# Optimization experiments

Hardware: AMD Instinct MI355X
Metric: run time of the kernel (lower is better)

Reference implementation:

```python
import jax, jax.numpy as jnp
import numpy as np

N, E, H, L, IN, OUT = 50000, 800000, 64, 14, 128, 112
MSG_EPS = 1e-7   # GENConv message epsilon
LN_EPS = 1e-5    # torch.nn.LayerNorm default eps


def setup_inputs() -> dict:
    key = jax.random.key(0)
    ks = jax.random.split(key, 8)
    s = 0.05
    x = jax.random.normal(ks[0], (N, IN), jnp.float32)
    edge_index = jax.random.randint(ks[1], (2, E), 0, N, dtype=jnp.int64)
    enc_W = jax.random.normal(ks[2], (IN, H), jnp.float32) * s
    enc_b = jnp.zeros((H,), jnp.float32)
    ln_g = jnp.ones((L, H), jnp.float32)
    ln_b = jnp.zeros((L, H), jnp.float32)
    mlp_W = jax.random.normal(ks[3], (L, H, H), jnp.float32) * s
    mlp_b = jnp.zeros((L, H), jnp.float32)
    pred_W = jax.random.normal(ks[4], (H, OUT), jnp.float32) * s
    pred_b = jnp.zeros((OUT,), jnp.float32)
    return dict(x=x, edge_index=edge_index, enc_W=enc_W, enc_b=enc_b,
                ln_g=ln_g, ln_b=ln_b, mlp_W=mlp_W, mlp_b=mlp_b,
                pred_W=pred_W, pred_b=pred_b)


def _layernorm(h, g, b):
    mu = jnp.mean(h, axis=-1, keepdims=True)
    var = jnp.mean(jnp.square(h - mu), axis=-1, keepdims=True)  # biased, as torch
    return (h - mu) * jax.lax.rsqrt(var + LN_EPS) * g + b


def _genconv(h, src, dst, W, b):
    # GENConv: msg = relu(x_src) + eps; softmax aggregation (t=1) over dst; out = Linear(x + agg)
    msg = jax.nn.relu(h[src]) + MSG_EPS                    # [E, H]
    mmax = jax.ops.segment_max(msg, dst, num_segments=N)   # [N, H]
    mmax = jnp.where(jnp.isfinite(mmax), mmax, 0.0)         # empty segments
    ex = jnp.exp(msg - mmax[dst])                           # [E, H]
    denom = jax.ops.segment_sum(ex, dst, num_segments=N)    # [N, H]
    num = jax.ops.segment_sum(msg * ex, dst, num_segments=N)
    agg = num / jnp.maximum(denom, 1e-16)                   # 0 for isolated nodes
    return (h + agg) @ W + b


def reference(x, edge_index, enc_W, enc_b, ln_g, ln_b, mlp_W, mlp_b, pred_W, pred_b):
    src, dst = edge_index[0], edge_index[1]
    h = x @ enc_W + enc_b                       # node feature encoder
    h = _genconv(h, src, dst, mlp_W[0], mlp_b[0])  # first GCN (no pre-norm in res+)

    def body(h, params):
        g, bl, W, b = params
        h2 = jax.nn.relu(_layernorm(h, g, bl))  # dropout is identity (eval)
        h = _genconv(h2, src, dst, W, b) + h    # residual
        return h, None

    h, _ = jax.lax.scan(body, h, (ln_g[:L - 1], ln_b[:L - 1], mlp_W[1:], mlp_b[1:]))
    return h @ pred_W + pred_b
```

## Files before the change

### kernel.cpp

```cpp
#include <hip/hip_runtime.h>
#include <hip/hip_bf16.h>

#define NN 50000
#define EE 800000
#define HD 64
#define LL 14
#define IND 128
#define OUTD 112
#define LN2 0.69314718056f

typedef __attribute__((ext_vector_type(8))) short short8;
typedef __attribute__((ext_vector_type(4))) float float4_;
typedef __attribute__((ext_vector_type(4))) unsigned short ushort4_;

__device__ __forceinline__ short bf16_hi(float x) {
    return (short)(__float_as_uint(x) >> 16);
}
__device__ __forceinline__ float bf16_f(short s) {
    return __uint_as_float(((unsigned)(unsigned short)s) << 16);
}
__device__ __forceinline__ unsigned short f2b_rne(float x) {
    unsigned u = __float_as_uint(x);
    u += 0x7fffu + ((u >> 16) & 1u);
    return (unsigned short)(u >> 16);
}

__device__ __forceinline__ void split8(const float* p, short8& hi, short8& lo) {
    float4_ a = *(const float4_*)p;
    float4_ b = *(const float4_*)(p + 4);
    float v[8] = {a[0], a[1], a[2], a[3], b[0], b[1], b[2], b[3]};
    #pragma unroll
    for (int j = 0; j < 8; ++j) {
        short h = bf16_hi(v[j]);
        hi[j] = h;
        lo[j] = bf16_hi(v[j] - bf16_f(h));
    }
}

__device__ __forceinline__ void load_b(const float* __restrict__ W, int ldw,
                                       int colbase, int krow, short8& hi, short8& lo) {
    #pragma unroll
    for (int j = 0; j < 8; ++j) {
        float wv = W[(krow + j) * ldw + colbase];
        short h = bf16_hi(wv);
        hi[j] = h;
        lo[j] = bf16_hi(wv - bf16_f(h));
    }
}

__device__ __forceinline__ float4_ mm3(short8 ah, short8 al, short8 bh, short8 bl,
                                       float4_ acc) {
    acc = __builtin_amdgcn_mfma_f32_16x16x32_bf16(ah, bh, acc, 0, 0, 0);
    acc = __builtin_amdgcn_mfma_f32_16x16x32_bf16(al, bh, acc, 0, 0, 0);
    acc = __builtin_amdgcn_mfma_f32_16x16x32_bf16(ah, bl, acc, 0, 0, 0);
    return acc;
}

#define ACCQ(q, sv, nv) { \
    float p0_ = __uint_as_float((q).x << 16); \
    float p1_ = __uint_as_float((q).x & 0xffff0000u); \
    float p2_ = __uint_as_float((q).y << 16); \
    float p3_ = __uint_as_float((q).y & 0xffff0000u); \
    sv[0] += p0_; sv[1] += p1_; sv[2] += p2_; sv[3] += p3_; \
    nv[0] = fmaf(p0_, __log2f(fmaxf(p0_, 1e-20f)), nv[0]); \
    nv[1] = fmaf(p1_, __log2f(fmaxf(p1_, 1e-20f)), nv[1]); \
    nv[2] = fmaf(p2_, __log2f(fmaxf(p2_, 1e-20f)), nv[2]); \
    nv[3] = fmaf(p3_, __log2f(fmaxf(p3_, 1e-20f)), nv[3]); }


__global__ void k_hist(const int* __restrict__ ei, int* __restrict__ cnt,
                       int* __restrict__ rank) {
    int e = blockIdx.x * blockDim.x + threadIdx.x;
    if (e < EE) rank[e] = atomicAdd(&cnt[ei[EE + e]], 1);
}

__global__ __launch_bounds__(1024) void k_scan1(const int* __restrict__ deg,
                                                int* __restrict__ excl,
                                                int* __restrict__ bsum) {
    __shared__ int ws[16];
    int tid = threadIdx.x, lane = tid & 63, w = tid >> 6;
    int gid = blockIdx.x * 1024 + tid;
    int v = (gid < NN) ? deg[gid] : 0;
    int x = v;
    #pragma unroll
    for (int d = 1; d < 64; d <<= 1) {
        int y = __shfl_up(x, d);
        if (lane >= d) x += y;
    }
    if (lane == 63) ws[w] = x;
    __syncthreads();
    if (tid == 0) {
        int acc = 0;
        for (int i = 0; i < 16; i++) { int t = ws[i]; ws[i] = acc; acc += t; }
        bsum[blockIdx.x] = acc;
    }
    __syncthreads();
    if (gid < NN) excl[gid] = x - v + ws[w];
}

__global__ void k_scan2(const int* __restrict__ bsum, int* __restrict__ boff, int nb) {
    if (threadIdx.x == 0) {
        int acc = 0;
        for (int i = 0; i < nb; i++) { boff[i] = acc; acc += bsum[i]; }
    }
}

__global__ __launch_bounds__(1024) void k_scan3(int* __restrict__ rp,
                                                const int* __restrict__ boff) {
    int gid = blockIdx.x * 1024 + threadIdx.x;
    if (gid < NN) rp[gid] += boff[blockIdx.x];
    if (gid == 0) rp[NN] = EE;
}

__global__ void k_scatter(const int* __restrict__ ei, const int* __restrict__ rp,
                          const int* __restrict__ rank, int* __restrict__ csrc) {
    int e = blockIdx.x * blockDim.x + threadIdx.x;
    if (e < EE) {
        int d = ei[EE + e];
        csrc[rp[d] + rank[e]] = ei[e];
    }
}


__global__ __launch_bounds__(256) void k_enc(const float* __restrict__ x,
                                             const float* __restrict__ W,
                                             const float* __restrict__ b,
                                             float* __restrict__ h,
                                             unsigned short* __restrict__ P0,
                                             unsigned short* __restrict__ P1) {
    __shared__ float X[16 * 132];
    int tid = threadIdx.x, lane = tid & 63, w = tid >> 6;
    int nb = blockIdx.x * 16;
    int nq = lane >> 4, nr = lane & 15;
    int colbase = w * 16 + nr;

    if (blockIdx.x == 0 && tid < HD) {
        P0[(size_t)NN * HD + tid] = 0;
        P1[(size_t)NN * HD + tid] = 0;
    }

    {
        const float* src = x + (size_t)nb * IND + tid * 8;
        float4_ a = *(const float4_*)src;
        float4_ c = *(const float4_*)(src + 4);
        int m = tid >> 4, k8 = 8 * (tid & 15);
        *(float4_*)&X[m * 132 + k8] = a;
        *(float4_*)&X[m * 132 + k8 + 4] = c;
    }
    __syncthreads();

    float4_ acc = {};
    #pragma unroll
    for (int t = 0; t < 4; ++t) {
        short8 ah, al, bh, bl;
        split8(&X[nr * 132 + t * 32 + nq * 8], ah, al);
        load_b(W, HD, colbase, t * 32 + nq * 8, bh, bl);
        acc = mm3(ah, al, bh, bl, acc);
    }

    float bias = b[colbase];
    #pragma unroll
    for (int r = 0; r < 4; ++r) {
        int node = nb + nq * 4 + r;
        float y = acc[r] + bias;
        h[node * HD + colbase] = y;
        float msg = fminf(fmaxf(y, 0.f) + 1e-7f, 50.f);
        P0[node * HD + colbase] = f2b_rne(__expf(msg));
    }
}

__device__ __forceinline__ void gtail(const unsigned* __restrict__ Pb,
                                      const int* __restrict__ csrc,
                                      int beg, int deg, int g, int co, int lane,
                                      float4_& sv, float4_& nv) {
    for (int chunk = 64; chunk < deg; chunk += 64) {
        int my = (chunk + lane < deg) ? csrc[beg + chunk + lane] : NN;
        int cnt = min(64, deg - chunk);
        int nb4 = (cnt + 3) >> 2;
        for (int k = 0; k < nb4; ++k) {
            int e = __shfl(my, k * 4 + g);
            uint2 q = *(const uint2*)(Pb + (((unsigned)e) << 5) + co);
            ACCQ(q, sv, nv);
        }
    }
}

__device__ __forceinline__ void finish_node(float4_ sv, float4_ nv, int node, int row,
                                            int g, int ci, int co,
                                            const float* __restrict__ selfh,
                                            const unsigned* __restrict__ Pb,
                                            uint2 selfq, float* __restrict__ T) {
    float t0 = sv[0], t1 = sv[1], t2 = sv[2], t3 = sv[3];
    float u0 = nv[0], u1 = nv[1], u2 = nv[2], u3 = nv[3];
    #pragma unroll
    for (int d = 16; d < 64; d <<= 1) {
        t0 += __shfl_xor(t0, d); t1 += __shfl_xor(t1, d);
        t2 += __shfl_xor(t2, d); t3 += __shfl_xor(t3, d);
        u0 += __shfl_xor(u0, d); u1 += __shfl_xor(u1, d);
        u2 += __shfl_xor(u2, d); u3 += __shfl_xor(u3, d);
    }
    if (g == 0) {
        float a0 = LN2 * u0 / fmaxf(t0, 1e-16f);
        float a1 = LN2 * u1 / fmaxf(t1, 1e-16f);
        float a2 = LN2 * u2 / fmaxf(t2, 1e-16f);
        float a3 = LN2 * u3 / fmaxf(t3, 1e-16f);
        float4_ xv;
        if (selfh) {
            float4_ sf = *(const float4_*)&selfh[(size_t)node * HD + ci * 4];
            xv[0] = sf[0] + a0; xv[1] = sf[1] + a1;
            xv[2] = sf[2] + a2; xv[3] = sf[3] + a3;
        } else {
            unsigned d0 = selfq.x, d1 = selfq.y;
            xv[0] = LN2 * __log2f(__uint_as_float(d0 << 16)) - 1e-7f + a0;
            xv[1] = LN2 * __log2f(__uint_as_float(d0 & 0xffff0000u)) - 1e-7f + a1;
            xv[2] = LN2 * __log2f(__uint_as_float(d1 << 16)) - 1e-7f + a2;
            xv[3] = LN2 * __log2f(__uint_as_float(d1 & 0xffff0000u)) - 1e-7f + a3;
        }
        *(float4_*)&T[row * 68 + ci * 4] = xv;
    }
}

__global__ __launch_bounds__(256, 4) void k_layer(const unsigned short* __restrict__ Pin,
                                                  const float* __restrict__ selfh,
                                                  const float* __restrict__ hres,
                                                  float* __restrict__ hout,
                                                  unsigned short* __restrict__ Pout,
                                                  const int* __restrict__ rp,
                                                  const int* __restrict__ csrc,
                                                  const float* __restrict__ W,
                                                  const float* __restrict__ b,
                                                  const float* __restrict__ gnext,
                                                  const float* __restrict__ bnext) {
    __shared__ float T[16 * 68];
    int tid = threadIdx.x, lane = tid & 63, w = tid >> 6;
    int nb = blockIdx.x * 16;
    int nq = lane >> 4, nr = lane & 15;
    int colbase = w * 16 + nr;

    short8 Bhi[2], Blo[2];
    #pragma unroll
    for (int t = 0; t < 2; ++t)
        load_b(W, HD, colbase, t * 32 + nq * 8, Bhi[t], Blo[t]);

    int g = lane >> 4;
    int ci = lane & 15;
    int co = ci << 1;
    int node0 = nb + w * 4;
    const unsigned* Pb = (const unsigned*)Pin;

    int r0 = rp[node0], r1 = rp[node0 + 1], r2 = rp[node0 + 2],
        r3 = rp[node0 + 3], r4 = rp[node0 + 4];
    int dA = r1 - r0, dB = r2 - r1, dC = r3 - r2, dD = r4 - r3;

    int myA = (lane < dA) ? csrc[r0 + lane] : NN;
    int myB = (lane < dB) ? csrc[r1 + lane] : NN;
    int myC = (lane < dC) ? csrc[r2 + lane] : NN;
    int myD = (lane < dD) ? csrc[r3 + lane] : NN;

    uint2 sq0 = {0, 0}, sq1 = {0, 0}, sq2 = {0, 0}, sq3 = {0, 0};
    if (!selfh) {
        sq0 = *(const uint2*)(Pb + (((unsigned)(node0 + 0)) << 5) + co);
        sq1 = *(const uint2*)(Pb + (((unsigned)(node0 + 1)) << 5) + co);
        sq2 = *(const uint2*)(Pb + (((unsigned)(node0 + 2)) << 5) + co);
        sq3 = *(const uint2*)(Pb + (((unsigned)(node0 + 3)) << 5) + co);
    }

    int cA = min(dA, 64), cB = min(dB, 64), cC = min(dC, 64), cD = min(dD, 64);
    int nk = (max(max(cA, cB), max(cC, cD)) + 3) >> 2;

    float4_ sA = {}, nA = {}, sB = {}, nB = {}, sC = {}, nC = {}, sD = {}, nD = {};

    #pragma unroll 2
    for (int k = 0; k < nk; ++k) {
        int sidx = k * 4 + g;
        int e0 = __shfl(myA, sidx);
        int e1 = __shfl(myB, sidx);
        int e2 = __shfl(myC, sidx);
        int e3 = __shfl(myD, sidx);
        uint2 q0 = *(const uint2*)(Pb + (((unsigned)e0) << 5) + co);
        uint2 q1 = *(const uint2*)(Pb + (((unsigned)e1) << 5) + co);
        uint2 q2 = *(const uint2*)(Pb + (((unsigned)e2) << 5) + co);
        uint2 q3 = *(const uint2*)(Pb + (((unsigned)e3) << 5) + co);
        ACCQ(q0, sA, nA);
        ACCQ(q1, sB, nB);
        ACCQ(q2, sC, nC);
        ACCQ(q3, sD, nD);
    }
    if (dA > 64) gtail(Pb, csrc, r0, dA, g, co, lane, sA, nA);
    if (dB > 64) gtail(Pb, csrc, r1, dB, g, co, lane, sB, nB);
    if (dC > 64) gtail(Pb, csrc, r2, dC, g, co, lane, sC, nC);
    if (dD > 64) gtail(Pb, csrc, r3, dD, g, co, lane, sD, nD);

    finish_node(sA, nA, node0 + 0, w * 4 + 0, g, ci, co, selfh, Pb, sq0, T);
    finish_node(sB, nB, node0 + 1, w * 4 + 1, g, ci, co, selfh, Pb, sq1, T);
    finish_node(sC, nC, node0 + 2, w * 4 + 2, g, ci, co, selfh, Pb, sq2, T);
    finish_node(sD, nD, node0 + 3, w * 4 + 3, g, ci, co, selfh, Pb, sq3, T);
    __syncthreads();

    short8 Ahi[2], Alo[2];
    #pragma unroll
    for (int t = 0; t < 2; ++t)
        split8(&T[nr * 68 + t * 32 + nq * 8], Ahi[t], Alo[t]);
    __syncthreads();

    float4_ acc = {};
    #pragma unroll
    for (int t = 0; t < 2; ++t)
        acc = mm3(Ahi[t], Alo[t], Bhi[t], Blo[t], acc);

    float bias = b[colbase];
    #pragma unroll
    for (int r = 0; r < 4; ++r) {
        int m = nq * 4 + r;
        int node = nb + m;
        float v = acc[r] + bias;
        if (hres) v += hres[node * HD + colbase];
        hout[node * HD + colbase] = v;
        T[m * 68 + colbase] = v;
    }
    if (!Pout) return;
    __syncthreads();

    int m = tid >> 4, c4 = (tid & 15) * 4;
    float4_ vv = *(const float4_*)&T[m * 68 + c4];
    float ps_ = (vv[0] + vv[1]) + (vv[2] + vv[3]);
    float pq_ = (vv[0] * vv[0] + vv[1] * vv[1]) + (vv[2] * vv[2] + vv[3] * vv[3]);
    #pragma unroll
    for (int d = 8; d; d >>= 1) {
        ps_ += __shfl_xor(ps_, d);
        pq_ += __shfl_xor(pq_, d);
    }
    float mu = ps_ * (1.f / 64.f);
    float var = pq_ * (1.f / 64.f) - mu * mu;
    float inv = rsqrtf(fmaxf(var, 0.f) + 1e-5f);
    float4_ g4 = *(const float4_*)&gnext[c4];
    float4_ b4 = *(const float4_*)&bnext[c4];
    ushort4_ po;
    #pragma unroll
    for (int j = 0; j < 4; ++j) {
        float y = fmaxf((vv[j] - mu) * inv * g4[j] + b4[j], 0.f);
        float msg = fminf(y + 1e-7f, 50.f);
        po[j] = f2b_rne(__expf(msg));
    }
    *(ushort4_*)&Pout[(nb + m) * HD + c4] = po;
}


__global__ __launch_bounds__(256) void k_pred(const float* __restrict__ h,
                                              const float* __restrict__ W,
                                              const float* __restrict__ b,
                                              float* __restrict__ out) {
    __shared__ float T[16 * 68];
    int tid = threadIdx.x, lane = tid & 63, w = tid >> 6;
    int nb = blockIdx.x * 16;
    int nq = lane >> 4, nr = lane & 15;

    {
        const float* src = h + (size_t)nb * HD + tid * 4;
        float4_ a = *(const float4_*)src;
        int m = tid >> 4, k4 = 4 * (tid & 15);
        *(float4_*)&T[m * 68 + k4] = a;
    }
    __syncthreads();

    short8 Ahi[2], Alo[2];
    #pragma unroll
    for (int t = 0; t < 2; ++t)
        split8(&T[nr * 68 + t * 32 + nq * 8], Ahi[t], Alo[t]);

    for (int tt = w; tt < 7; tt += 4) {
        int colbase = tt * 16 + nr;
        float4_ acc = {};
        #pragma unroll
        for (int t = 0; t < 2; ++t) {
            short8 bh, bl;
            load_b(W, OUTD, colbase, t * 32 + nq * 8, bh, bl);
            acc = mm3(Ahi[t], Alo[t], bh, bl, acc);
        }
        float bias = b[colbase];
        #pragma unroll
        for (int r = 0; r < 4; ++r) {
            int node = nb + nq * 4 + r;
            out[node * OUTD + colbase] = acc[r] + bias;
        }
    }
}


extern "C" void kernel_launch(void* const* d_in, const int* in_sizes, int n_in,
                              void* d_out, int out_size, void* d_ws, size_t ws_size,
                              hipStream_t stream) {
    const float* x    = (const float*)d_in[0];
    const int*   ei   = (const int*)d_in[1];
    const float* encW = (const float*)d_in[2];
    const float* encb = (const float*)d_in[3];
    const float* lng  = (const float*)d_in[4];
    const float* lnb  = (const float*)d_in[5];
    const float* mlpW = (const float*)d_in[6];
    const float* mlpb = (const float*)d_in[7];
    const float* pW   = (const float*)d_in[8];
    const float* pb   = (const float*)d_in[9];
    float* out = (float*)d_out;

    float* hA  = (float*)d_ws;
    float* hB  = hA + (size_t)NN * HD;
    unsigned short* PA = (unsigned short*)(hB + (size_t)NN * HD);
    unsigned short* PB = PA + (size_t)(NN + 1) * HD;
    int* rp   = (int*)(PB + (size_t)(NN + 1) * HD);
    int* cnt  = rp + (NN + 1);
    int* csrc = cnt + NN;
    int* rank = csrc + EE;
    int* bsum = rank + EE;
    int* boff = bsum + 64;

    hipMemsetAsync(cnt, 0, NN * sizeof(int), stream);
    k_hist<<<(EE + 255) / 256, 256, 0, stream>>>(ei, cnt, rank);
    const int NB = (NN + 1023) / 1024;
    k_scan1<<<NB, 1024, 0, stream>>>(cnt, rp, bsum);
    k_scan2<<<1, 64, 0, stream>>>(bsum, boff, NB);
    k_scan3<<<NB, 1024, 0, stream>>>(rp, boff);
    k_scatter<<<(EE + 255) / 256, 256, 0, stream>>>(ei, rp, rank, csrc);

    k_enc<<<NN / 16, 256, 0, stream>>>(x, encW, encb, hA, PA, PB);

    k_layer<<<NN / 16, 256, 0, stream>>>(PA, hA, nullptr, hB, PB, rp, csrc,
                                         mlpW, mlpb, lng, lnb);

    float* hres = hB;
    float* hdst = hA;
    unsigned short* pc = PB;
    unsigned short* pn = PA;
    for (int l = 1; l < LL; ++l) {
        bool last = (l == LL - 1);
        k_layer<<<NN / 16, 256, 0, stream>>>(pc, nullptr, hres, hdst,
                                             last ? nullptr : pn,
                                             rp, csrc,
                                             mlpW + (size_t)l * HD * HD,
                                             mlpb + (size_t)l * HD,
                                             last ? nullptr : lng + (size_t)l * HD,
                                             last ? nullptr : lnb + (size_t)l * HD);
        float* t = hres; hres = hdst; hdst = t;
        unsigned short* u = pc; pc = pn; pn = u;
    }

    k_pred<<<NN / 16, 256, 0, stream>>>(hres, pW, pb, out);
}
```

Measured before the change: 696.7 us.

## Sort nodes by in-degree to balance per-wave gather work

Adds a counting-sort pass (histogram, scan, scatter) that orders nodes by in-degree, capped at 63, into a descriptor array. Each layer wave then processes four nodes of similar degree, so lanes waste fewer iterations padding to the largest degree in the group. The padding sentinel row now holds exp(0)=1, so the log guard can be dropped, and that padding is subtracted from the denominator. The block-offset scan also becomes a wave shuffle scan. In exchange, outputs are written through an indirect node index, so stores scatter instead of being contiguous, and three small setup kernels are added.

Result: faster. 671.3 us (-3.7%).

```diff
diff --git a/kernel.cpp b/kernel.cpp
--- a/kernel.cpp
+++ b/kernel.cpp
@@ -62,10 +62,10 @@
     float p2_ = __uint_as_float((q).y << 16); \
     float p3_ = __uint_as_float((q).y & 0xffff0000u); \
     sv[0] += p0_; sv[1] += p1_; sv[2] += p2_; sv[3] += p3_; \
-    nv[0] = fmaf(p0_, __log2f(fmaxf(p0_, 1e-20f)), nv[0]); \
-    nv[1] = fmaf(p1_, __log2f(fmaxf(p1_, 1e-20f)), nv[1]); \
-    nv[2] = fmaf(p2_, __log2f(fmaxf(p2_, 1e-20f)), nv[2]); \
-    nv[3] = fmaf(p3_, __log2f(fmaxf(p3_, 1e-20f)), nv[3]); }
+    nv[0] = fmaf(p0_, __log2f(p0_), nv[0]); \
+    nv[1] = fmaf(p1_, __log2f(p1_), nv[1]); \
+    nv[2] = fmaf(p2_, __log2f(p2_), nv[2]); \
+    nv[3] = fmaf(p3_, __log2f(p3_), nv[3]); }
 
 
 __global__ void k_hist(const int* __restrict__ ei, int* __restrict__ cnt,
@@ -99,10 +99,15 @@
 }
 
 __global__ void k_scan2(const int* __restrict__ bsum, int* __restrict__ boff, int nb) {
-    if (threadIdx.x == 0) {
-        int acc = 0;
-        for (int i = 0; i < nb; i++) { boff[i] = acc; acc += bsum[i]; }
-    }
+    int lane = threadIdx.x & 63;
+    int v = (lane < nb) ? bsum[lane] : 0;
+    int x = v;
+    #pragma unroll
+    for (int d = 1; d < 64; d <<= 1) {
+        int y = __shfl_up(x, d);
+        if (lane >= d) x += y;
+    }
+    if (lane < nb) boff[lane] = x - v;
 }
 
 __global__ __launch_bounds__(1024) void k_scan3(int* __restrict__ rp,
@@ -118,6 +123,54 @@
     if (e < EE) {
         int d = ei[EE + e];
         csrc[rp[d] + rank[e]] = ei[e];
+    }
+}
+
+
+__global__ __launch_bounds__(256) void k_dhist(const int* __restrict__ deg,
+                                               int* __restrict__ bhist) {
+    __shared__ int lh[64];
+    int tid = threadIdx.x;
+    if (tid < 64) lh[tid] = 0;
+    __syncthreads();
+    int n = blockIdx.x * 256 + tid;
+    if (n < NN) atomicAdd(&lh[min(deg[n], 63)], 1);
+    __syncthreads();
+    if (tid < 64 && lh[tid]) atomicAdd(&bhist[tid], lh[tid]);
+}
+
+__global__ void k_dscan(const int* __restrict__ bhist, int* __restrict__ gboff) {
+    int lane = threadIdx.x & 63;
+    int v = bhist[lane];
+    int x = v;
+    #pragma unroll
+    for (int d = 1; d < 64; d <<= 1) {
+        int y = __shfl_up(x, d);
+        if (lane >= d) x += y;
+    }
+    gboff[lane] = x - v;
+}
+
+__global__ __launch_bounds__(256) void k_dscatter(const int* __restrict__ deg,
+                                                  const int* __restrict__ rp,
+                                                  int* __restrict__ gboff,
+                                                  int4* __restrict__ nd) {
+    __shared__ int lh[64], lbase[64];
+    int tid = threadIdx.x;
+    if (tid < 64) lh[tid] = 0;
+    __syncthreads();
+    int n = blockIdx.x * 256 + tid;
+    int b = 0, lr = 0;
+    if (n < NN) {
+        b = min(deg[n], 63);
+        lr = atomicAdd(&lh[b], 1);
+    }
+    __syncthreads();
+    if (tid < 64) lbase[tid] = lh[tid] ? atomicAdd(&gboff[tid], lh[tid]) : 0;
+    __syncthreads();
+    if (n < NN) {
+        int pos = lbase[b] + lr;
+        nd[pos] = make_int4(n, rp[n], rp[n + 1] - rp[n], 0);
     }
 }
 
@@ -135,8 +188,8 @@
     int colbase = w * 16 + nr;
 
     if (blockIdx.x == 0 && tid < HD) {
-        P0[(size_t)NN * HD + tid] = 0;
-        P1[(size_t)NN * HD + tid] = 0;
+        P0[(size_t)NN * HD + tid] = 0x3f80;
+        P1[(size_t)NN * HD + tid] = 0x3f80;
     }
 
     {
@@ -172,11 +225,12 @@
 __device__ __forceinline__ void gtail(const unsigned* __restrict__ Pb,
                                       const int* __restrict__ csrc,
                                       int beg, int deg, int g, int co, int lane,
-                                      float4_& sv, float4_& nv) {
+                                      float4_& sv, float4_& nv, int& waste) {
     for (int chunk = 64; chunk < deg; chunk += 64) {
         int my = (chunk + lane < deg) ? csrc[beg + chunk + lane] : NN;
         int cnt = min(64, deg - chunk);
         int nb4 = (cnt + 3) >> 2;
+        waste += nb4 * 4 - cnt;
         for (int k = 0; k < nb4; ++k) {
             int e = __shfl(my, k * 4 + g);
             uint2 q = *(const uint2*)(Pb + (((unsigned)e) << 5) + co);
@@ -185,10 +239,9 @@
     }
 }
 
-__device__ __forceinline__ void finish_node(float4_ sv, float4_ nv, int node, int row,
-                                            int g, int ci, int co,
+__device__ __forceinline__ void finish_node(float4_ sv, float4_ nv, int waste,
+                                            int pnode, int row, int g, int ci,
                                             const float* __restrict__ selfh,
-                                            const unsigned* __restrict__ Pb,
                                             uint2 selfq, float* __restrict__ T) {
     float t0 = sv[0], t1 = sv[1], t2 = sv[2], t3 = sv[3];
     float u0 = nv[0], u1 = nv[1], u2 = nv[2], u3 = nv[3];
@@ -200,13 +253,14 @@
         u2 += __shfl_xor(u2, d); u3 += __shfl_xor(u3, d);
     }
     if (g == 0) {
-        float a0 = LN2 * u0 / fmaxf(t0, 1e-16f);
-        float a1 = LN2 * u1 / fmaxf(t1, 1e-16f);
-        float a2 = LN2 * u2 / fmaxf(t2, 1e-16f);
-        float a3 = LN2 * u3 / fmaxf(t3, 1e-16f);
+        float wf = (float)waste;
+        float a0 = LN2 * u0 / fmaxf(t0 - wf, 1e-16f);
+        float a1 = LN2 * u1 / fmaxf(t1 - wf, 1e-16f);
+        float a2 = LN2 * u2 / fmaxf(t2 - wf, 1e-16f);
+        float a3 = LN2 * u3 / fmaxf(t3 - wf, 1e-16f);
         float4_ xv;
         if (selfh) {
-            float4_ sf = *(const float4_*)&selfh[(size_t)node * HD + ci * 4];
+            float4_ sf = *(const float4_*)&selfh[(size_t)pnode * HD + ci * 4];
             xv[0] = sf[0] + a0; xv[1] = sf[1] + a1;
             xv[2] = sf[2] + a2; xv[3] = sf[3] + a3;
         } else {
@@ -225,18 +279,21 @@
                                                   const float* __restrict__ hres,
                                                   float* __restrict__ hout,
                                                   unsigned short* __restrict__ Pout,
-                                                  const int* __restrict__ rp,
+                                                  const int4* __restrict__ nd,
                                                   const int* __restrict__ csrc,
                                                   const float* __restrict__ W,
                                                   const float* __restrict__ b,
                                                   const float* __restrict__ gnext,
                                                   const float* __restrict__ bnext) {
     __shared__ float T[16 * 68];
+    __shared__ int PN[16];
     int tid = threadIdx.x, lane = tid & 63, w = tid >> 6;
     int nb = blockIdx.x * 16;
     int nq = lane >> 4, nr = lane & 15;
     int colbase = w * 16 + nr;
 
+    if (tid < 16) PN[tid] = nd[nb + tid].x;
+
     short8 Bhi[2], Blo[2];
     #pragma unroll
     for (int t = 0; t < 2; ++t)
@@ -245,12 +302,16 @@
     int g = lane >> 4;
     int ci = lane & 15;
     int co = ci << 1;
-    int node0 = nb + w * 4;
     const unsigned* Pb = (const unsigned*)Pin;
 
-    int r0 = rp[node0], r1 = rp[node0 + 1], r2 = rp[node0 + 2],
-        r3 = rp[node0 + 3], r4 = rp[node0 + 4];
-    int dA = r1 - r0, dB = r2 - r1, dC = r3 - r2, dD = r4 - r3;
+    int4 dsc0 = nd[nb + w * 4 + 0];
+    int4 dsc1 = nd[nb + w * 4 + 1];
+    int4 dsc2 = nd[nb + w * 4 + 2];
+    int4 dsc3 = nd[nb + w * 4 + 3];
+    int p0n = dsc0.x, r0 = dsc0.y, dA = dsc0.z;
+    int p1n = dsc1.x, r1 = dsc1.y, dB = dsc1.z;
+    int p2n = dsc2.x, r2 = dsc2.y, dC = dsc2.z;
+    int p3n = dsc3.x, r3 = dsc3.y, dD = dsc3.z;
 
     int myA = (lane < dA) ? csrc[r0 + lane] : NN;
     int myB = (lane < dB) ? csrc[r1 + lane] : NN;
@@ -259,14 +320,15 @@
 
     uint2 sq0 = {0, 0}, sq1 = {0, 0}, sq2 = {0, 0}, sq3 = {0, 0};
     if (!selfh) {
-        sq0 = *(const uint2*)(Pb + (((unsigned)(node0 + 0)) << 5) + co);
-        sq1 = *(const uint2*)(Pb + (((unsigned)(node0 + 1)) << 5) + co);
-        sq2 = *(const uint2*)(Pb + (((unsigned)(node0 + 2)) << 5) + co);
-        sq3 = *(const uint2*)(Pb + (((unsigned)(node0 + 3)) << 5) + co);
+        sq0 = *(const uint2*)(Pb + (((unsigned)p0n) << 5) + co);
+        sq1 = *(const uint2*)(Pb + (((unsigned)p1n) << 5) + co);
+        sq2 = *(const uint2*)(Pb + (((unsigned)p2n) << 5) + co);
+        sq3 = *(const uint2*)(Pb + (((unsigned)p3n) << 5) + co);
     }
 
     int cA = min(dA, 64), cB = min(dB, 64), cC = min(dC, 64), cD = min(dD, 64);
     int nk = (max(max(cA, cB), max(cC, cD)) + 3) >> 2;
+    int wA = nk * 4 - cA, wB = nk * 4 - cB, wC = nk * 4 - cC, wD = nk * 4 - cD;
 
     float4_ sA = {}, nA = {}, sB = {}, nB = {}, sC = {}, nC = {}, sD = {}, nD = {};
 
@@ -286,15 +348,15 @@
         ACCQ(q2, sC, nC);
         ACCQ(q3, sD, nD);
     }
-    if (dA > 64) gtail(Pb, csrc, r0, dA, g, co, lane, sA, nA);
-    if (dB > 64) gtail(Pb, csrc, r1, dB, g, co, lane, sB, nB);
-    if (dC > 64) gtail(Pb, csrc, r2, dC, g, co, lane, sC, nC);
-    if (dD > 64) gtail(Pb, csrc, r3, dD, g, co, lane, sD, nD);
-
-    finish_node(sA, nA, node0 + 0, w * 4 + 0, g, ci, co, selfh, Pb, sq0, T);
-    finish_node(sB, nB, node0 + 1, w * 4 + 1, g, ci, co, selfh, Pb, sq1, T);
-    finish_node(sC, nC, node0 + 2, w * 4 + 2, g, ci, co, selfh, Pb, sq2, T);
-    finish_node(sD, nD, node0 + 3, w * 4 + 3, g, ci, co, selfh, Pb, sq3, T);
+    if (dA > 64) gtail(Pb, csrc, r0, dA, g, co, lane, sA, nA, wA);
+    if (dB > 64) gtail(Pb, csrc, r1, dB, g, co, lane, sB, nB, wB);
+    if (dC > 64) gtail(Pb, csrc, r2, dC, g, co, lane, sC, nC, wC);
+    if (dD > 64) gtail(Pb, csrc, r3, dD, g, co, lane, sD, nD, wD);
+
+    finish_node(sA, nA, wA, p0n, w * 4 + 0, g, ci, selfh, sq0, T);
+    finish_node(sB, nB, wB, p1n, w * 4 + 1, g, ci, selfh, sq1, T);
+    finish_node(sC, nC, wC, p2n, w * 4 + 2, g, ci, selfh, sq2, T);
+    finish_node(sD, nD, wD, p3n, w * 4 + 3, g, ci, selfh, sq3, T);
     __syncthreads();
 
     short8 Ahi[2], Alo[2];
@@ -312,10 +374,10 @@
     #pragma unroll
     for (int r = 0; r < 4; ++r) {
         int m = nq * 4 + r;
-        int node = nb + m;
+        int pn = PN[m];
         float v = acc[r] + bias;
-        if (hres) v += hres[node * HD + colbase];
-        hout[node * HD + colbase] = v;
+        if (hres) v += hres[pn * HD + colbase];
+        hout[pn * HD + colbase] = v;
         T[m * 68 + colbase] = v;
     }
     if (!Pout) return;
@@ -342,7 +404,7 @@
         float msg = fminf(y + 1e-7f, 50.f);
         po[j] = f2b_rne(__expf(msg));
     }
-    *(ushort4_*)&Pout[(nb + m) * HD + c4] = po;
+    *(ushort4_*)&Pout[(size_t)PN[m] * HD + c4] = po;
 }
 
 
@@ -402,18 +464,22 @@
     const float* pb   = (const float*)d_in[9];
     float* out = (float*)d_out;
 
-    float* hA  = (float*)d_ws;
+    int4* nd = (int4*)d_ws;
+    float* hA  = (float*)(nd + NN);
     float* hB  = hA + (size_t)NN * HD;
     unsigned short* PA = (unsigned short*)(hB + (size_t)NN * HD);
     unsigned short* PB = PA + (size_t)(NN + 1) * HD;
-    int* rp   = (int*)(PB + (size_t)(NN + 1) * HD);
-    int* cnt  = rp + (NN + 1);
-    int* csrc = cnt + NN;
-    int* rank = csrc + EE;
-    int* bsum = rank + EE;
-    int* boff = bsum + 64;
+    int* rp    = (int*)(PB + (size_t)(NN + 1) * HD);
+    int* cnt   = rp + (NN + 1);
+    int* csrc  = cnt + NN;
+    int* rank  = csrc + EE;
+    int* bsum  = rank + EE;
+    int* boff  = bsum + 64;
+    int* bhist = boff + 64;
+    int* gboff = bhist + 64;
 
     hipMemsetAsync(cnt, 0, NN * sizeof(int), stream);
+    hipMemsetAsync(bhist, 0, 64 * sizeof(int), stream);
     k_hist<<<(EE + 255) / 256, 256, 0, stream>>>(ei, cnt, rank);
     const int NB = (NN + 1023) / 1024;
     k_scan1<<<NB, 1024, 0, stream>>>(cnt, rp, bsum);
@@ -421,9 +487,14 @@
     k_scan3<<<NB, 1024, 0, stream>>>(rp, boff);
     k_scatter<<<(EE + 255) / 256, 256, 0, stream>>>(ei, rp, rank, csrc);
 
+    const int NDB = (NN + 255) / 256;
+    k_dhist<<<NDB, 256, 0, stream>>>(cnt, bhist);
+    k_dscan<<<1, 64, 0, stream>>>(bhist, gboff);
+    k_dscatter<<<NDB, 256, 0, stream>>>(cnt, rp, gboff, nd);
+
     k_enc<<<NN / 16, 256, 0, stream>>>(x, encW, encb, hA, PA, PB);
 
-    k_layer<<<NN / 16, 256, 0, stream>>>(PA, hA, nullptr, hB, PB, rp, csrc,
+    k_layer<<<NN / 16, 256, 0, stream>>>(PA, hA, nullptr, hB, PB, nd, csrc,
                                          mlpW, mlpb, lng, lnb);
 
     float* hres = hB;
@@ -434,7 +505,7 @@
         bool last = (l == LL - 1);
         k_layer<<<NN / 16, 256, 0, stream>>>(pc, nullptr, hres, hdst,
                                              last ? nullptr : pn,
-                                             rp, csrc,
+                                             nd, csrc,
                                              mlpW + (size_t)l * HD * HD,
                                              mlpb + (size_t)l * HD,
                                              last ? nullptr : lng + (size_t)l * HD,
```
